# Kernel optimization log

Hardware: AMD Instinct MI355X
Metric: run time of the kernel (lower is better)

## Reference

```python
import jax, jax.numpy as jnp
import numpy as np

N_ATT, N_HEAD, D_K, D_IN = 4, 8, 64, 512
B, T = 128, 512
TEMP = float(np.sqrt(D_K))  # temperature = d_k ** 0.5


def setup_inputs() -> dict:
    key = jax.random.key(0)
    k1, k2, k3 = jax.random.split(key, 3)
    v = jax.random.normal(k1, (B, T, D_IN), jnp.float32)
    # nn.Parameter Q init: normal(0, sqrt(2/d_k))
    Q = jax.random.normal(k2, (N_ATT, N_HEAD, D_K), jnp.float32) * np.sqrt(2.0 / D_K)
    # fc1_k: Linear(d_in, num_attention*n_head*d_k), weight ~ N(0, sqrt(2/d_k))
    Wk = jax.random.normal(k3, (N_ATT * N_HEAD * D_K, D_IN), jnp.float32) * np.sqrt(2.0 / D_K)
    bk = jnp.zeros((N_ATT * N_HEAD * D_K,), jnp.float32)
    return {"v": v, "Q": Q, "Wk": Wk, "bk": bk}


def reference(v, Q, Wk, bk):
    A, H, dk = Q.shape
    Bsz, Tt, d_in = v.shape
    c = d_in // H  # per-head value channels

    # q = stack(Q, dim=2 over batch).view(-1, d_k)  -> [A*H*B, d_k]
    q = jnp.broadcast_to(Q[:, :, None, :], (A, H, Bsz, dk)).reshape(-1, dk)

    # k = fc1_k(v).view(B,T,A,H,dk).permute(3,0,1,2,4).contiguous().view(-1,T,dk)
    # NOTE: this view is a raw C-order reinterpretation (scrambles t/A axes);
    # transpose + reshape reproduces torch's contiguous().view() exactly.
    k = (v @ Wk.T + bk).reshape(Bsz, Tt, A, H, dk)
    k = jnp.transpose(k, (3, 0, 1, 2, 4)).reshape(-1, Tt, dk)  # [H*B*A, T, dk]

    # v heads: stack(v.split(c, dim=-1)).view(H*B, T, c)
    vh = jnp.transpose(v.reshape(Bsz, Tt, H, c), (2, 0, 1, 3)).reshape(H * Bsz, Tt, c)

    # single-query scaled dot-product attention (dropout in eval mode -> identity)
    attn = jnp.einsum('xd,xtd->xt', q, k) / TEMP  # [A*H*B, T]
    attn = jax.nn.softmax(attn, axis=-1)

    # v[:, None].expand(-1, A, -1, -1).reshape(-1, T, c)
    vexp = jnp.broadcast_to(vh[:, None], (H * Bsz, A, Tt, c)).reshape(-1, Tt, c)
    out = jnp.einsum('xt,xtc->xc', attn, vexp)  # [A*H*B, c]

    output = out.reshape(A, H, Bsz, c)
    attn = attn.reshape(A, H, Bsz, Tt)
    return output, attn
```

## Files before the change

kernel.cpp:

```cpp
#include <hip/hip_runtime.h>
#include <hip/hip_bf16.h>
#include <math.h>

#define DIN 512
#define TT  512
#define BSZ 128

using bf16x8 = __attribute__((ext_vector_type(8))) short;
using f32x4  = __attribute__((ext_vector_type(4))) float;

static __device__ __forceinline__ unsigned short f2bf(float x) {
    __hip_bfloat16 h = __float2bfloat16(x);
    return *reinterpret_cast<unsigned short*>(&h);
}
static __device__ __forceinline__ unsigned int pack2(float a, float b) {
    return (unsigned int)f2bf(a) | ((unsigned int)f2bf(b) << 16);
}


__global__ __launch_bounds__(512) void pk_kernel(const float* __restrict__ Q,
                                                 const float* __restrict__ Wk,
                                                 const float* __restrict__ bk,
                                                 unsigned short* __restrict__ Pgb,
                                                 float* __restrict__ qb) {
    const int bid = blockIdx.x;
    const int bg = bid >> 5;
    const int p  = bid & 31;
    const int h  = p >> 2;
    const int ua = p & 3;
    const int a_q = h >> 1;
    const int h_q = (4 * h + bg) & 7;
    const int ch_base = ua * 512 + h * 64;

    __shared__ float qv[64];
    const int tid = threadIdx.x;
    if (tid < 64) qv[tid] = Q[(a_q * 8 + h_q) * 64 + tid];
    __syncthreads();

    const int s = tid;
    float acc = 0.f;
    #pragma unroll 8
    for (int d = 0; d < 64; ++d)
        acc += qv[d] * Wk[(size_t)(ch_base + d) * DIN + s];
    Pgb[(size_t)(bg * 32 + p) * 512 + s] = f2bf(acc * 0.125f);

    if (tid == 0) {
        float sum = 0.f;
        for (int d = 0; d < 64; ++d) sum += qv[d] * bk[ch_base + d];
        qb[bg * 32 + p] = sum * 0.125f;
    }
}

__global__ __launch_bounds__(256) void score_kernel(const float* __restrict__ v,
                                                    const unsigned short* __restrict__ Pgb,
                                                    const float* __restrict__ qb,
                                                    float* __restrict__ attn) {
    const int bid = blockIdx.x;
    const int b = bid >> 2;
    const int j = bid & 3;
    const int bg = b >> 5;
    const int tid = threadIdx.x;
    const int lane = tid & 63;
    const int w = tid >> 6;

    __shared__ char VtB[128 * 80];
    __shared__ char PtB[32 * 1040];
    __shared__ float red2[4][2][4][2];

    const float* vbase = v + ((size_t)b * TT + j * 128) * DIN;

    {
        const int p  = tid >> 3;
        const int sg = tid & 7;
        const uint4* src = (const uint4*)(Pgb + ((size_t)(bg * 32 + p) * 512)) + sg * 8;
        uint4* dst = (uint4*)(PtB + p * 1040 + sg * 128);
        #pragma unroll
        for (int q = 0; q < 8; ++q) dst[q] = src[q];
    }

    const float qv0 = qb[bg * 32 + (lane & 15)];
    const float qv1 = qb[bg * 32 + 16 + (lane & 15)];

    f32x4 acc[2][2];
    #pragma unroll
    for (int i = 0; i < 2; ++i)
        #pragma unroll
        for (int n = 0; n < 2; ++n)
            #pragma unroll
            for (int r = 0; r < 4; ++r) acc[i][n][r] = 0.f;

    const int srow  = tid >> 1;
    const int shalf = tid & 1;
    const float* vsrc = vbase + (size_t)srow * DIN + shalf * 16;
    char* vdst = VtB + srow * 80 + shalf * 32;

    const int akb = (lane >> 4) * 16;
    const char* aptr = VtB + (w * 32 + (lane & 15)) * 80 + akb;
    const char* bptr0 = PtB + ((lane & 15)) * 1040 + akb;
    const char* bptr1 = PtB + (16 + (lane & 15)) * 1040 + akb;

    float4 vr[4];
    #pragma unroll
    for (int q = 0; q < 4; ++q) vr[q] = *(const float4*)(vsrc + q * 4);

    for (int kt = 0; kt < 16; ++kt) {
        uint4 lo, hi;
        lo.x = pack2(vr[0].x, vr[0].y); lo.y = pack2(vr[0].z, vr[0].w);
        lo.z = pack2(vr[1].x, vr[1].y); lo.w = pack2(vr[1].z, vr[1].w);
        hi.x = pack2(vr[2].x, vr[2].y); hi.y = pack2(vr[2].z, vr[2].w);
        hi.z = pack2(vr[3].x, vr[3].y); hi.w = pack2(vr[3].z, vr[3].w);
        *(uint4*)(vdst)      = lo;
        *(uint4*)(vdst + 16) = hi;
        __syncthreads();

        if (kt < 15) {
            const float* vn = vsrc + (kt + 1) * 32;
            #pragma unroll
            for (int q = 0; q < 4; ++q) vr[q] = *(const float4*)(vn + q * 4);
        }

        const int ksb = kt * 64;
        bf16x8 a0 = *(const bf16x8*)(aptr);
        bf16x8 a1 = *(const bf16x8*)(aptr + 16 * 80);
        bf16x8 b0 = *(const bf16x8*)(bptr0 + ksb);
        bf16x8 b1 = *(const bf16x8*)(bptr1 + ksb);
        acc[0][0] = __builtin_amdgcn_mfma_f32_16x16x32_bf16(a0, b0, acc[0][0], 0, 0, 0);
        acc[0][1] = __builtin_amdgcn_mfma_f32_16x16x32_bf16(a0, b1, acc[0][1], 0, 0, 0);
        acc[1][0] = __builtin_amdgcn_mfma_f32_16x16x32_bf16(a1, b0, acc[1][0], 0, 0, 0);
        acc[1][1] = __builtin_amdgcn_mfma_f32_16x16x32_bf16(a1, b1, acc[1][1], 0, 0, 0);
        __syncthreads();
    }

    float lg[2][8];
    #pragma unroll
    for (int i = 0; i < 2; ++i)
        #pragma unroll
        for (int r = 0; r < 4; ++r) {
            lg[0][i * 4 + r] = acc[i][0][r] + qv0;
            lg[1][i * 4 + r] = acc[i][1][r] + qv1;
        }

    const int hsub = (lane >> 2) & 3;
    float mw[2], sw[2], ev[2][8];
    #pragma unroll
    for (int nt = 0; nt < 2; ++nt) {
        float m = lg[nt][0];
        #pragma unroll
        for (int q = 1; q < 8; ++q) m = fmaxf(m, lg[nt][q]);
        m = fmaxf(m, __shfl_xor(m, 1));
        m = fmaxf(m, __shfl_xor(m, 2));
        m = fmaxf(m, __shfl_xor(m, 16));
        m = fmaxf(m, __shfl_xor(m, 32));
        float s = 0.f;
        #pragma unroll
        for (int q = 0; q < 8; ++q) { ev[nt][q] = __expf(lg[nt][q] - m); s += ev[nt][q]; }
        s += __shfl_xor(s, 1);
        s += __shfl_xor(s, 2);
        s += __shfl_xor(s, 16);
        s += __shfl_xor(s, 32);
        mw[nt] = m; sw[nt] = s;
    }
    if ((lane & 0x33) == 0) {
        #pragma unroll
        for (int nt = 0; nt < 2; ++nt) {
            red2[w][nt][hsub][0] = mw[nt];
            red2[w][nt][hsub][1] = sw[nt];
        }
    }
    __syncthreads();

    #pragma unroll
    for (int nt = 0; nt < 2; ++nt) {
        float M = red2[0][nt][hsub][0];
        M = fmaxf(M, red2[1][nt][hsub][0]);
        M = fmaxf(M, red2[2][nt][hsub][0]);
        M = fmaxf(M, red2[3][nt][hsub][0]);
        float S = 0.f;
        #pragma unroll
        for (int w2 = 0; w2 < 4; ++w2)
            S += __expf(red2[w2][nt][hsub][0] - M) * red2[w2][nt][hsub][1];
        const float factor = __expf(mw[nt] - M) / S;

        const int h = nt * 4 + hsub;
        float* arow = attn + ((size_t)(h * 512 + b * 4 + j)) * 512;
        const int ua = lane & 3;
        #pragma unroll
        for (int i = 0; i < 2; ++i)
            #pragma unroll
            for (int r = 0; r < 4; ++r) {
                const int trow = w * 32 + i * 16 + ((lane >> 4) & 3) * 4 + r;
                arow[trow * 4 + ua] = ev[nt][i * 4 + r] * factor;
            }
    }
}

__global__ __launch_bounds__(256) void pv_kernel(const float* __restrict__ v,
                                                 const float* __restrict__ attn,
                                                 float* __restrict__ out) {
    const int bid = blockIdx.x;
    const int b = bid >> 3;
    const int h = bid & 7;
    const int tid = threadIdx.x;

    __shared__ float at[4][512];
    __shared__ float red[32][4][68];

    {
        const int j  = tid >> 6;
        const int u8 = (tid & 63) * 8;
        const float* src = attn + ((size_t)(h * 512 + b * 4 + j)) * 512 + u8;
        *(float4*)&at[j][u8]     = *(const float4*)(src);
        *(float4*)&at[j][u8 + 4] = *(const float4*)(src + 4);
    }
    __syncthreads();

    const int cg = tid & 7;
    const int up = tid >> 3;
    const int c8 = cg * 8;
    const float* vb = v + (size_t)b * TT * DIN + h * 64 + c8;

    float acc[4][8];
    #pragma unroll
    for (int jj = 0; jj < 4; ++jj)
        #pragma unroll
        for (int ci = 0; ci < 8; ++ci) acc[jj][ci] = 0.f;

    const float* pcur = vb + (size_t)up * DIN;
    float4 r0 = *(const float4*)(pcur);
    float4 r1 = *(const float4*)(pcur + 4);

    for (int it = 0; it < 16; ++it) {
        const int u = it * 32 + up;
        const float4 c0 = r0;
        const float4 c1 = r1;
        if (it < 15) {
            const float* pn = vb + (size_t)(u + 32) * DIN;
            r0 = *(const float4*)(pn);
            r1 = *(const float4*)(pn + 4);
        }
        const float a0 = at[0][u];
        const float a1 = at[1][u];
        const float a2 = at[2][u];
        const float a3 = at[3][u];
        acc[0][0] += a0 * c0.x; acc[0][1] += a0 * c0.y; acc[0][2] += a0 * c0.z; acc[0][3] += a0 * c0.w;
        acc[0][4] += a0 * c1.x; acc[0][5] += a0 * c1.y; acc[0][6] += a0 * c1.z; acc[0][7] += a0 * c1.w;
        acc[1][0] += a1 * c0.x; acc[1][1] += a1 * c0.y; acc[1][2] += a1 * c0.z; acc[1][3] += a1 * c0.w;
        acc[1][4] += a1 * c1.x; acc[1][5] += a1 * c1.y; acc[1][6] += a1 * c1.z; acc[1][7] += a1 * c1.w;
        acc[2][0] += a2 * c0.x; acc[2][1] += a2 * c0.y; acc[2][2] += a2 * c0.z; acc[2][3] += a2 * c0.w;
        acc[2][4] += a2 * c1.x; acc[2][5] += a2 * c1.y; acc[2][6] += a2 * c1.z; acc[2][7] += a2 * c1.w;
        acc[3][0] += a3 * c0.x; acc[3][1] += a3 * c0.y; acc[3][2] += a3 * c0.z; acc[3][3] += a3 * c0.w;
        acc[3][4] += a3 * c1.x; acc[3][5] += a3 * c1.y; acc[3][6] += a3 * c1.z; acc[3][7] += a3 * c1.w;
    }

    #pragma unroll
    for (int jj = 0; jj < 4; ++jj) {
        float4 w0, w1;
        w0.x = acc[jj][0]; w0.y = acc[jj][1]; w0.z = acc[jj][2]; w0.w = acc[jj][3];
        w1.x = acc[jj][4]; w1.y = acc[jj][5]; w1.z = acc[jj][6]; w1.w = acc[jj][7];
        *(float4*)&red[up][jj][c8]     = w0;
        *(float4*)&red[up][jj][c8 + 4] = w1;
    }
    __syncthreads();

    const int jo = tid >> 6;
    const int c  = tid & 63;
    float s = 0.f;
    #pragma unroll
    for (int r2 = 0; r2 < 32; ++r2) s += red[r2][jo][c];
    out[((size_t)(h * 512 + b * 4 + jo)) * 64 + c] = s;
}

extern "C" void kernel_launch(void* const* d_in, const int* in_sizes, int n_in,
                              void* d_out, int out_size, void* d_ws, size_t ws_size,
                              hipStream_t stream) {
    const float* v  = (const float*)d_in[0];
    const float* Q  = (const float*)d_in[1];
    const float* Wk = (const float*)d_in[2];
    const float* bk = (const float*)d_in[3];

    float* out  = (float*)d_out;
    float* attn = out + 4096 * 64;

    unsigned short* Pgb = (unsigned short*)d_ws;
    float* qb = (float*)(Pgb + 4 * 32 * 512);

    pk_kernel<<<128, 512, 0, stream>>>(Q, Wk, bk, Pgb, qb);
    score_kernel<<<512, 256, 0, stream>>>(v, Pgb, qb, attn);
    pv_kernel<<<1024, 256, 0, stream>>>(v, attn, out);
}
```

Baseline: 56.43 us.

## Double-buffer V tile in score kernel, load P from global, alias pv smem

The score kernel stops staging the projected-key matrix P in shared memory and loads its bf16 fragments straight from global into registers, prefetched one k-step ahead. The V tile is double-buffered in LDS so the next tile's conversion and store overlap the current MFMAs, cutting two barriers per step to one. The pv kernel aliases its attention and reduction shared arrays into one buffer, adding a barrier between uses. Together these shrink LDS use to allow higher occupancy, at the cost of more registers and repeated global reads of P.

```diff
diff --git a/kernel.cpp b/kernel.cpp
--- a/kernel.cpp
+++ b/kernel.cpp
@@ -4,7 +4,6 @@
 
 #define DIN 512
 #define TT  512
-#define BSZ 128
 
 using bf16x8 = __attribute__((ext_vector_type(8))) short;
 using f32x4  = __attribute__((ext_vector_type(4))) float;
@@ -63,20 +62,20 @@
     const int lane = tid & 63;
     const int w = tid >> 6;
 
-    __shared__ char VtB[128 * 80];
-    __shared__ char PtB[32 * 1040];
+    __shared__ __align__(16) char VtB[2][128 * 80];
     __shared__ float red2[4][2][4][2];
 
     const float* vbase = v + ((size_t)b * TT + j * 128) * DIN;
-
-    {
-        const int p  = tid >> 3;
-        const int sg = tid & 7;
-        const uint4* src = (const uint4*)(Pgb + ((size_t)(bg * 32 + p) * 512)) + sg * 8;
-        uint4* dst = (uint4*)(PtB + p * 1040 + sg * 128);
-        #pragma unroll
-        for (int q = 0; q < 8; ++q) dst[q] = src[q];
-    }
+    const int srow  = tid >> 1;
+    const int shalf = tid & 1;
+    const float* vsrc = vbase + (size_t)srow * DIN + shalf * 16;
+    const int vdo = srow * 80 + shalf * 32;
+
+    const unsigned short* pb0 = Pgb + ((size_t)(bg * 32) + (lane & 15)) * 512 + (lane >> 4) * 8;
+    const unsigned short* pb1 = pb0 + 16 * 512;
+
+    const int akb = (lane >> 4) * 16;
+    const int aoff = (w * 32 + (lane & 15)) * 80 + akb;
 
     const float qv0 = qb[bg * 32 + (lane & 15)];
     const float qv1 = qb[bg * 32 + 16 + (lane & 15)];
@@ -89,47 +88,57 @@
             #pragma unroll
             for (int r = 0; r < 4; ++r) acc[i][n][r] = 0.f;
 
-    const int srow  = tid >> 1;
-    const int shalf = tid & 1;
-    const float* vsrc = vbase + (size_t)srow * DIN + shalf * 16;
-    char* vdst = VtB + srow * 80 + shalf * 32;
-
-    const int akb = (lane >> 4) * 16;
-    const char* aptr = VtB + (w * 32 + (lane & 15)) * 80 + akb;
-    const char* bptr0 = PtB + ((lane & 15)) * 1040 + akb;
-    const char* bptr1 = PtB + (16 + (lane & 15)) * 1040 + akb;
-
-    float4 vr[4];
-    #pragma unroll
-    for (int q = 0; q < 4; ++q) vr[q] = *(const float4*)(vsrc + q * 4);
-
-    for (int kt = 0; kt < 16; ++kt) {
+    float4 vrA[4], vrB[4];
+    bf16x8 brA0, brA1, brB0, brB1;
+    #pragma unroll
+    for (int q = 0; q < 4; ++q) vrA[q] = *(const float4*)(vsrc + q * 4);
+    brA0 = *(const bf16x8*)(pb0);
+    brA1 = *(const bf16x8*)(pb1);
+    {
         uint4 lo, hi;
-        lo.x = pack2(vr[0].x, vr[0].y); lo.y = pack2(vr[0].z, vr[0].w);
-        lo.z = pack2(vr[1].x, vr[1].y); lo.w = pack2(vr[1].z, vr[1].w);
-        hi.x = pack2(vr[2].x, vr[2].y); hi.y = pack2(vr[2].z, vr[2].w);
-        hi.z = pack2(vr[3].x, vr[3].y); hi.w = pack2(vr[3].z, vr[3].w);
-        *(uint4*)(vdst)      = lo;
-        *(uint4*)(vdst + 16) = hi;
-        __syncthreads();
-
-        if (kt < 15) {
-            const float* vn = vsrc + (kt + 1) * 32;
-            #pragma unroll
-            for (int q = 0; q < 4; ++q) vr[q] = *(const float4*)(vn + q * 4);
-        }
-
-        const int ksb = kt * 64;
-        bf16x8 a0 = *(const bf16x8*)(aptr);
-        bf16x8 a1 = *(const bf16x8*)(aptr + 16 * 80);
-        bf16x8 b0 = *(const bf16x8*)(bptr0 + ksb);
-        bf16x8 b1 = *(const bf16x8*)(bptr1 + ksb);
-        acc[0][0] = __builtin_amdgcn_mfma_f32_16x16x32_bf16(a0, b0, acc[0][0], 0, 0, 0);
-        acc[0][1] = __builtin_amdgcn_mfma_f32_16x16x32_bf16(a0, b1, acc[0][1], 0, 0, 0);
-        acc[1][0] = __builtin_amdgcn_mfma_f32_16x16x32_bf16(a1, b0, acc[1][0], 0, 0, 0);
-        acc[1][1] = __builtin_amdgcn_mfma_f32_16x16x32_bf16(a1, b1, acc[1][1], 0, 0, 0);
-        __syncthreads();
-    }
+        lo.x = pack2(vrA[0].x, vrA[0].y); lo.y = pack2(vrA[0].z, vrA[0].w);
+        lo.z = pack2(vrA[1].x, vrA[1].y); lo.w = pack2(vrA[1].z, vrA[1].w);
+        hi.x = pack2(vrA[2].x, vrA[2].y); hi.y = pack2(vrA[2].z, vrA[2].w);
+        hi.z = pack2(vrA[3].x, vrA[3].y); hi.w = pack2(vrA[3].z, vrA[3].w);
+        *(uint4*)(VtB[0] + vdo)      = lo;
+        *(uint4*)(VtB[0] + vdo + 16) = hi;
+    }
+    __syncthreads();
+
+#define STEP(CUR, VRN, BRC0, BRC1, BRN0, BRN1, KT)                            \
+    {                                                                         \
+        if ((KT) + 1 < 16) {                                                  \
+            const float* vn = vsrc + ((KT) + 1) * 32;                         \
+            VRN[0] = *(const float4*)(vn);                                    \
+            VRN[1] = *(const float4*)(vn + 4);                                \
+            VRN[2] = *(const float4*)(vn + 8);                                \
+            VRN[3] = *(const float4*)(vn + 12);                               \
+            BRN0 = *(const bf16x8*)(pb0 + ((KT) + 1) * 32);                   \
+            BRN1 = *(const bf16x8*)(pb1 + ((KT) + 1) * 32);                   \
+        }                                                                     \
+        bf16x8 a0 = *(const bf16x8*)(VtB[CUR] + aoff);                        \
+        bf16x8 a1 = *(const bf16x8*)(VtB[CUR] + aoff + 16 * 80);              \
+        acc[0][0] = __builtin_amdgcn_mfma_f32_16x16x32_bf16(a0, BRC0, acc[0][0], 0, 0, 0); \
+        acc[0][1] = __builtin_amdgcn_mfma_f32_16x16x32_bf16(a0, BRC1, acc[0][1], 0, 0, 0); \
+        acc[1][0] = __builtin_amdgcn_mfma_f32_16x16x32_bf16(a1, BRC0, acc[1][0], 0, 0, 0); \
+        acc[1][1] = __builtin_amdgcn_mfma_f32_16x16x32_bf16(a1, BRC1, acc[1][1], 0, 0, 0); \
+        if ((KT) + 1 < 16) {                                                  \
+            uint4 lo, hi;                                                     \
+            lo.x = pack2(VRN[0].x, VRN[0].y); lo.y = pack2(VRN[0].z, VRN[0].w); \
+            lo.z = pack2(VRN[1].x, VRN[1].y); lo.w = pack2(VRN[1].z, VRN[1].w); \
+            hi.x = pack2(VRN[2].x, VRN[2].y); hi.y = pack2(VRN[2].z, VRN[2].w); \
+            hi.z = pack2(VRN[3].x, VRN[3].y); hi.w = pack2(VRN[3].z, VRN[3].w); \
+            *(uint4*)(VtB[(CUR) ^ 1] + vdo)      = lo;                        \
+            *(uint4*)(VtB[(CUR) ^ 1] + vdo + 16) = hi;                        \
+        }                                                                     \
+        __syncthreads();                                                      \
+    }
+
+    for (int kt = 0; kt < 16; kt += 2) {
+        STEP(0, vrB, brA0, brA1, brB0, brB1, kt)
+        STEP(1, vrA, brB0, brB1, brA0, brA1, kt + 1)
+    }
+#undef STEP
 
     float lg[2][8];
     #pragma unroll
@@ -202,8 +211,9 @@
     const int h = bid & 7;
     const int tid = threadIdx.x;
 
-    __shared__ float at[4][512];
-    __shared__ float red[32][4][68];
+    __shared__ __align__(16) char smem[34816];
+    float (*at)[512]    = reinterpret_cast<float (*)[512]>(smem);
+    float (*red)[4][68] = reinterpret_cast<float (*)[4][68]>(smem);
 
     {
         const int j  = tid >> 6;
@@ -225,9 +235,8 @@
         #pragma unroll
         for (int ci = 0; ci < 8; ++ci) acc[jj][ci] = 0.f;
 
-    const float* pcur = vb + (size_t)up * DIN;
-    float4 r0 = *(const float4*)(pcur);
-    float4 r1 = *(const float4*)(pcur + 4);
+    float4 r0 = *(const float4*)(vb + (size_t)up * DIN);
+    float4 r1 = *(const float4*)(vb + (size_t)up * DIN + 4);
 
     for (int it = 0; it < 16; ++it) {
         const int u = it * 32 + up;
@@ -252,6 +261,8 @@
         acc[3][4] += a3 * c1.x; acc[3][5] += a3 * c1.y; acc[3][6] += a3 * c1.z; acc[3][7] += a3 * c1.w;
     }
 
+    __syncthreads();
+
     #pragma unroll
     for (int jj = 0; jj < 4; ++jj) {
         float4 w0, w1;
```

Result: slower. 59.17 us (+4.9%).
